# Kernel optimization log

Hardware: AMD Instinct MI355X
Metric: run time of the kernel (lower is better)

The kernel has to match this reference:

```python
import jax, jax.numpy as jnp
import numpy as np

N_QUBITS = 6
N_LAYERS = 2
QSVT_DEGREE = 3
DT_RANK = max(N_QUBITS // 2, 1)
OUT_DIM = 3 * N_QUBITS
PI = np.float32(np.pi)
DT_MIN, DT_MAX = 1e-3, 0.1
BATCH, SEQ = 256, 512


def _ry_mat(theta):
    c = jnp.cos(theta / 2)
    s = jnp.sin(theta / 2)
    row0 = jnp.stack([c, -s], axis=-1)
    row1 = jnp.stack([s, c], axis=-1)
    return jnp.stack([row0, row1], axis=-2).astype(jnp.complex64)


def _rz_mat(theta):
    e = jnp.exp(-0.5j * theta.astype(jnp.complex64))
    z = jnp.zeros_like(e)
    row0 = jnp.stack([e, z], axis=-1)
    row1 = jnp.stack([z, jnp.conj(e)], axis=-1)
    return jnp.stack([row0, row1], axis=-2)


def _rx_mat(theta):
    c = jnp.cos(theta / 2).astype(jnp.complex64)
    s = jnp.sin(theta / 2).astype(jnp.complex64)
    row0 = jnp.stack([c, -1j * s], axis=-1)
    row1 = jnp.stack([-1j * s, c], axis=-1)
    return jnp.stack([row0, row1], axis=-2)


def _apply1(state, mat, w):
    # state: (B, 2, ..., 2) tensor over N_QUBITS axes; mat: (2,2) or batched (B,2,2)
    state = jnp.moveaxis(state, 1 + w, -1)
    if mat.ndim == 3:
        state = jnp.einsum('bij,b...j->b...i', mat, state)
    else:
        state = jnp.einsum('ij,b...j->b...i', mat, state)
    return jnp.moveaxis(state, -1, 1 + w)


def _cnot(state, c, t):
    state = jnp.moveaxis(state, (1 + c, 1 + t), (-2, -1))
    state = state.at[..., 1, :].set(state[..., 1, ::-1])
    return jnp.moveaxis(state, (-2, -1), (1 + c, 1 + t))


def _crx(state, theta, c, t):
    state = jnp.moveaxis(state, (1 + c, 1 + t), (-2, -1))
    m = _rx_mat(theta)
    state = state.at[..., 1, :].set(jnp.einsum('ij,...j->...i', m, state[..., 1, :]))
    return jnp.moveaxis(state, (-2, -1), (1 + c, 1 + t))


def _circuit(h, x, dt, circuit_params, poly_coeffs, qsvt_params):
    """Batched statevector simulation of the selective QSVT + unified ansatz qnode."""
    n = N_QUBITS
    B = h.shape[0]
    state = jnp.zeros((B,) + (2,) * n, jnp.complex64)
    state = state.at[(slice(None),) + (0,) * n].set(1.0 + 0.0j)
    # 1) state encoding RY(h[t-1])
    for i in range(n):
        state = _apply1(state, _ry_mat(h[:, i]), i)
    # 2) Delta-modulated QSVT: RZ rotations + bidirectional CNOT ring per degree
    qidx = 0
    n_qp = n * QSVT_DEGREE
    for deg in range(QSVT_DEGREE + 1):
        coeff = poly_coeffs[deg]
        for i in range(n):
            if qidx < n_qp:
                ang = coeff * dt[:, i] * qsvt_params[qidx] * PI
                qidx += 1
            else:
                ang = coeff * dt[:, i] * PI
            state = _apply1(state, _rz_mat(ang), i)
        for i in range(n - 1):
            state = _cnot(state, i, i + 1)
        state = _cnot(state, n - 1, 0)
        for i in range(n - 1, 0, -1):
            state = _cnot(state, i, i - 1)
    # 3) unified variational ansatz
    p = 0
    for _ in range(N_LAYERS):
        for i in range(n):
            state = _apply1(state, _rx_mat(circuit_params[p]), i)
            state = _apply1(state, _ry_mat(circuit_params[p + 1]), i)
            state = _apply1(state, _rz_mat(circuit_params[p + 2]), i)
            p += 3
        for i in range(n):
            state = _crx(state, circuit_params[p], i, (i + 1) % n)
            p += 1
        for i in range(n - 1, -1, -1):
            state = _crx(state, circuit_params[p], i, (i - 1) % n)
            p += 1
    # 4) Delta-modulated input RY(x * dt)
    for i in range(n):
        state = _apply1(state, _ry_mat(x[:, i] * dt[:, i]), i)
    # 5) Pauli X/Y/Z expectation values per qubit
    xs, ys, zs = [], [], []
    for i in range(n):
        s = jnp.moveaxis(state, 1 + i, 1).reshape(B, 2, -1)
        z = jnp.sum(jnp.conj(s[:, 0]) * s[:, 1], axis=-1)
        xs.append(2.0 * jnp.real(z))
        ys.append(2.0 * jnp.imag(z))
        zs.append(jnp.sum(jnp.abs(s[:, 0]) ** 2 - jnp.abs(s[:, 1]) ** 2, axis=-1))
    return jnp.stack(xs + ys + zs, axis=-1).astype(jnp.float32)  # (B, 3n)


def setup_inputs() -> dict:
    key = jax.random.key(0)
    ks = jax.random.split(key, 8)
    angles = jax.random.uniform(ks[0], (BATCH, SEQ, N_QUBITS), jnp.float32) * PI
    Wx = jax.random.normal(ks[1], (DT_RANK + 2 * N_QUBITS, N_QUBITS), jnp.float32) / np.float32(np.sqrt(N_QUBITS))
    Wdt = jax.random.normal(ks[2], (N_QUBITS, DT_RANK), jnp.float32) / np.float32(np.sqrt(DT_RANK))
    dt = jnp.exp(jax.random.uniform(ks[3], (N_QUBITS,), jnp.float32) * np.float32(np.log(DT_MAX) - np.log(DT_MIN)) + np.float32(np.log(DT_MIN)))
    bdt = dt + jnp.log(-jnp.expm1(-dt))
    poly_coeffs = jax.random.normal(ks[4], (QSVT_DEGREE + 1,), jnp.float32) * 0.1
    qsvt_params = jax.random.normal(ks[5], (N_QUBITS * QSVT_DEGREE,), jnp.float32) * 0.1
    circuit_params = jax.random.normal(ks[6], (5 * N_QUBITS * N_LAYERS,), jnp.float32) * 0.1
    D = jnp.ones((OUT_DIM,), jnp.float32)
    Wc = jax.random.normal(ks[7], (OUT_DIM, N_QUBITS), jnp.float32) / np.float32(np.sqrt(N_QUBITS))
    return {"angles": angles, "Wx": Wx, "Wdt": Wdt, "bdt": bdt, "poly_coeffs": poly_coeffs, "qsvt_params": qsvt_params, "circuit_params": circuit_params, "D": D, "Wc": Wc}


def reference(angles, Wx, Wdt, bdt, poly_coeffs, qsvt_params, circuit_params, D, Wc):
    x_dbc = angles @ Wx.T  # (B,S, dt_rank + 2n)
    dt_raw = x_dbc[..., :DT_RANK]
    # B slice computed in the original but never used in forward
    C = x_dbc[..., DT_RANK + N_QUBITS:]
    dt_angles = jnp.tanh(jax.nn.softplus(dt_raw @ Wdt.T + bdt)) * PI  # (B,S,n)
    # quantum part is detached in the original (detach().cpu() before the qnode)
    sg = jax.lax.stop_gradient
    xs = (jnp.moveaxis(sg(angles), 1, 0), jnp.moveaxis(sg(dt_angles), 1, 0))
    cp, pc, qp = sg(circuit_params), sg(poly_coeffs), sg(qsvt_params)
    h0 = jnp.zeros((angles.shape[0], N_QUBITS), jnp.float32)

    def step(h, xt):
        x_t, dt_t = xt
        meas = _circuit(h, x_t, dt_t, cp, pc, qp)
        return meas[:, 2 * N_QUBITS:], meas  # carry = PauliZ block

    _, meas = jax.lax.scan(step, h0, xs)
    h_full = jnp.moveaxis(meas, 0, 1)  # (B,S,3n)
    return (C @ Wc.T) * h_full + D * jnp.concatenate([angles] * 3, axis=-1)
```

## Files before the change

### kernel.cpp

```cpp
#include <hip/hip_runtime.h>
#include <math.h>

#define BATCH 256
#define SEQ 512
#define SDS 54
#define PI_F 3.14159265358979323846f

template<int CTRL>
__device__ __forceinline__ float fdpp(float v) {
    return __int_as_float(__builtin_amdgcn_mov_dpp(__float_as_int(v), CTRL, 0xF, 0xF, true));
}
template<int L>
__device__ __forceinline__ float rdl(float v) {
    return __int_as_float(__builtin_amdgcn_readlane(__float_as_int(v), L));
}
__device__ __forceinline__ float rdlv(float v, int l) {
    return __int_as_float(__builtin_amdgcn_readlane(__float_as_int(v), l));
}
template<int M>
__device__ __forceinline__ float shxm(float v) {
    if constexpr (M == 1)       return fdpp<0xB1>(v);
    else if constexpr (M == 2)  return fdpp<0x4E>(v);
    else if constexpr (M == 8)  return fdpp<0x128>(v);
    else if constexpr (M == 32) return __shfl_xor(v, 32, 64);
    else return __int_as_float(__builtin_amdgcn_ds_swizzle(__float_as_int(v), (M << 10) | 0x1F));
}
__device__ __forceinline__ float redsum64(float v) {
    v += fdpp<0x128>(v);
    v += fdpp<0x124>(v);
    v += fdpp<0x122>(v);
    v += fdpp<0x121>(v);
    return (rdl<0>(v) + rdl<16>(v)) + (rdl<32>(v) + rdl<48>(v));
}
__device__ __forceinline__ float xorf(float v, int m) {
    return __int_as_float(__float_as_int(v) ^ m);
}
__device__ __forceinline__ void wg_barrier_lds() {
    __builtin_amdgcn_sched_barrier(0);
    __builtin_amdgcn_s_waitcnt(0xC07F);
    __builtin_amdgcn_s_barrier();
    __builtin_amdgcn_sched_barrier(0);
}
__device__ __forceinline__ int permf(int x) {
    const int cs[11] = {0,1,2,3,4,5,5,4,3,2,1};
    const int ts[11] = {1,2,3,4,5,0,4,3,2,1,0};
#pragma unroll
    for (int k = 10; k >= 0; k--) {
        int cb = (x >> (5 - cs[k])) & 1;
        x ^= cb << (5 - ts[k]);
    }
    return x;
}
__device__ __forceinline__ void cmul4(const float* c,
    float vr, float vi, float ar, float ai, float br, float bi, float cr, float ci,
    float& nr, float& ni) {
    nr = c[0]*vr - c[1]*vi + c[2]*ar - c[3]*ai + c[4]*br - c[5]*bi + c[6]*cr - c[7]*ci;
    ni = c[0]*vi + c[1]*vr + c[2]*ai + c[3]*ar + c[4]*bi + c[5]*br + c[6]*ci + c[7]*cr;
}
__device__ __forceinline__ void ringapply(const float* rc,
    float vr, float vi, float br, float bi, float cr, float ci, float dr, float di,
    float& nr, float& ni) {
    nr = rc[0]*vr - rc[1]*bi - rc[2]*ci + rc[3]*dr;
    ni = rc[0]*vi + rc[1]*br + rc[2]*cr + rc[3]*di;
}

__global__ __launch_bounds__(256) void prep_kernel(
    const float* __restrict__ angles, const float* __restrict__ Wx,
    const float* __restrict__ Wdt, const float* __restrict__ bdt,
    const float* __restrict__ D, const float* __restrict__ Wc,
    float* __restrict__ sd)
{
    int gid = blockIdx.x * blockDim.x + threadIdx.x;
    if (gid >= BATCH * SEQ) return;
    const float* a = angles + (size_t)gid * 6;
    float ang[6];
#pragma unroll
    for (int i = 0; i < 6; i++) ang[i] = a[i];
    float dtr[3];
#pragma unroll
    for (int r = 0; r < 3; r++) {
        float s = 0.f;
#pragma unroll
        for (int k = 0; k < 6; k++) s += ang[k] * Wx[r * 6 + k];
        dtr[r] = s;
    }
    float* rec = sd + (size_t)gid * SDS;
    float dtv[6];
#pragma unroll
    for (int i = 0; i < 6; i++) {
        float x = bdt[i];
#pragma unroll
        for (int r = 0; r < 3; r++) x += dtr[r] * Wdt[i * 3 + r];
        float sp = (x > 15.f) ? x : log1pf(expf(x));
        dtv[i] = tanhf(sp) * PI_F;
        rec[i] = dtv[i];
        float th = ang[i] * dtv[i];
        rec[6 + i]  = cosf(th);
        rec[12 + i] = sinf(th);
    }
    float C[6];
#pragma unroll
    for (int i = 0; i < 6; i++) {
        float s = 0.f;
#pragma unroll
        for (int k = 0; k < 6; k++) s += ang[k] * Wx[(9 + i) * 6 + k];
        C[i] = s;
    }
#pragma unroll
    for (int j = 0; j < 18; j++) {
        float s = 0.f;
#pragma unroll
        for (int i = 0; i < 6; i++) s += C[i] * Wc[j * 6 + i];
        rec[18 + j] = s;
        rec[36 + j] = D[j] * ang[j % 6];
    }
}

__global__ __launch_bounds__(64) void umat_kernel(const float* __restrict__ cp,
                                                  float2* __restrict__ um)
{
    const int lane = threadIdx.x;
    const int col = blockIdx.x;
    int bitv[6];
#pragma unroll
    for (int i = 0; i < 6; i++) bitv[i] = (lane >> (5 - i)) & 1;

    float qc[2][3][8], rc[2][6][4];
#pragma unroll
    for (int l = 0; l < 2; l++) {
        float g00r[6], g00i[6], g01r[6], g01i[6], g10r[6], g10i[6], g11r[6], g11i[6];
#pragma unroll
        for (int i = 0; i < 6; i++) {
            float ax = cp[l * 30 + i * 3 + 0];
            float ay = cp[l * 30 + i * 3 + 1];
            float az = cp[l * 30 + i * 3 + 2];
            float ca = cosf(0.5f * ax), sa = sinf(0.5f * ax);
            float cb = cosf(0.5f * ay), sb = sinf(0.5f * ay);
            float cg = cosf(0.5f * az), sg = sinf(0.5f * az);
            float m00r = cb * ca, m00i =  sb * sa;
            float m01r = -sb * ca, m01i = -cb * sa;
            float m10r =  sb * ca, m10i = -cb * sa;
            float m11r =  cb * ca, m11i = -sb * sa;
            g00r[i] = cg * m00r + sg * m00i; g00i[i] = cg * m00i - sg * m00r;
            g01r[i] = cg * m01r + sg * m01i; g01i[i] = cg * m01i - sg * m01r;
            g10r[i] = cg * m10r - sg * m10i; g10i[i] = cg * m10i + sg * m10r;
            g11r[i] = cg * m11r - sg * m11i; g11i[i] = cg * m11i + sg * m11r;
        }
#pragma unroll
        for (int pp = 0; pp < 3; pp++) {
            int aq = 2 * pp, bq = 2 * pp + 1;
            float dar = bitv[aq] ? g11r[aq] : g00r[aq], dai = bitv[aq] ? g11i[aq] : g00i[aq];
            float oar = bitv[aq] ? g10r[aq] : g01r[aq], oai = bitv[aq] ? g10i[aq] : g01i[aq];
            float dbr = bitv[bq] ? g11r[bq] : g00r[bq], dbi = bitv[bq] ? g11i[bq] : g00i[bq];
            float obr = bitv[bq] ? g10r[bq] : g01r[bq], obi = bitv[bq] ? g10i[bq] : g01i[bq];
            qc[l][pp][0] = dar * dbr - dai * dbi;  qc[l][pp][1] = dar * dbi + dai * dbr;
            qc[l][pp][2] = oar * dbr - oai * dbi;  qc[l][pp][3] = oar * dbi + oai * dbr;
            qc[l][pp][4] = dar * obr - dai * obi;  qc[l][pp][5] = dar * obi + dai * obr;
            qc[l][pp][6] = oar * obr - oai * obi;  qc[l][pp][7] = oar * obi + oai * obr;
        }
        const int Aq[6] = {0, 2, 4, 5, 3, 1};
        const int Bq[6] = {1, 3, 5, 4, 2, 0};
#pragma unroll
        for (int o = 0; o < 6; o++) {
            float tha = (o < 3) ? cp[l * 30 + 18 + 2 * o]     : cp[l * 30 + 24 + 2 * (o - 3)];
            float thb = (o < 3) ? cp[l * 30 + 18 + 2 * o + 1] : cp[l * 30 + 24 + 2 * (o - 3) + 1];
            float ca = cosf(0.5f * tha), sa = sinf(0.5f * tha);
            float cb = cosf(0.5f * thb), sb = sinf(0.5f * thb);
            int ba = bitv[Aq[o]], bb = bitv[Bq[o]];
            float mx0 = ba ? ca : 1.f, sae = ba ? sa : 0.f;
            float ny0 = bb ? cb : 1.f, sbe = bb ? sb : 0.f;
            rc[l][o][0] = ny0 * mx0; rc[l][o][1] = -ny0 * sae;
            rc[l][o][2] = -mx0 * sbe; rc[l][o][3] = -sae * sbe;
        }
    }

    float re = (lane == col) ? 1.f : 0.f;
    float im = 0.f;
    auto p1q = [&](int mi, int mj, const float* c) {
        float ar = __shfl_xor(re, mi, 64), ai = __shfl_xor(im, mi, 64);
        float br = __shfl_xor(re, mj, 64), bi = __shfl_xor(im, mj, 64);
        float cr = __shfl_xor(re, mi | mj, 64), ci = __shfl_xor(im, mi | mj, 64);
        float nr, ni;
        cmul4(c, re, im, ar, ai, br, bi, cr, ci, nr, ni);
        re = nr; im = ni;
    };
    auto rng = [&](int mb, int mc, const float* c) {
        float br = __shfl_xor(re, mb, 64), bi = __shfl_xor(im, mb, 64);
        float cr = __shfl_xor(re, mc, 64), ci = __shfl_xor(im, mc, 64);
        float dr = __shfl_xor(re, mb | mc, 64), di = __shfl_xor(im, mb | mc, 64);
        float nr, ni;
        ringapply(c, re, im, br, bi, cr, ci, dr, di, nr, ni);
        re = nr; im = ni;
    };
#pragma unroll
    for (int l = 0; l < 2; l++) {
        p1q(32, 16, qc[l][0]);
        p1q(8, 4, qc[l][1]);
        p1q(2, 1, qc[l][2]);
        rng(16, 8, rc[l][0]);
        rng(4, 2, rc[l][1]);
        rng(1, 32, rc[l][2]);
        rng(2, 4, rc[l][3]);
        rng(8, 16, rc[l][4]);
        rng(32, 1, rc[l][5]);
    }
    um[(size_t)lane * 64 + col] = make_float2(re, im);
}

__global__ __launch_bounds__(256, 1) void step_kernel(
    const float* __restrict__ sd, const float* __restrict__ pc,
    const float* __restrict__ qp, const float2* __restrict__ um,
    float* __restrict__ out)
{
    __shared__ float2 sPart[2][4][64];
    const int tid = threadIdx.x;
    const int wave = tid >> 6;
    const int lane = tid & 63;
    const int b = blockIdx.x;

    int bitv[6];
#pragma unroll
    for (int i = 0; i < 6; i++) bitv[i] = (lane >> (5 - i)) & 1;
    int sflip[6];
#pragma unroll
    for (int q = 0; q < 6; q++) sflip[q] = bitv[q] ? (int)0x80000000 : 0;

    const int jbase = wave * 16;
    float2 row[16];
#pragma unroll
    for (int jj = 0; jj < 16; jj++) row[jj] = um[(size_t)lane * 64 + jbase + jj];

    float A[6], sel[6];
    {
        int x1 = permf(lane), x2 = permf(x1), x3 = permf(x2), x4 = permf(x3);
#pragma unroll
        for (int i = 0; i < 6; i++) {
            float u0 = pc[0] * PI_F * qp[0 * 6 + i];
            float u1 = pc[1] * PI_F * qp[1 * 6 + i];
            float u2 = pc[2] * PI_F * qp[2 * 6 + i];
            float u3 = pc[3] * PI_F;
            float t1 = ((x1 >> (5 - i)) & 1) ? 0.5f : -0.5f;
            float t2 = ((x2 >> (5 - i)) & 1) ? 0.5f : -0.5f;
            float t3 = ((x3 >> (5 - i)) & 1) ? 0.5f : -0.5f;
            float t4 = ((x4 >> (5 - i)) & 1) ? 0.5f : -0.5f;
            A[i] = u3 * t1 + u2 * t2 + u1 * t3 + u0 * t4;
            sel[i] = (float)((x4 >> (5 - i)) & 1);
        }
    }

    const float* sdb = sd + (size_t)b * SEQ * SDS;
    float* outb = out + (size_t)b * SEQ * 18;

    float h0 = 0.f, h1 = 0.f, h2 = 0.f, h3 = 0.f, h4 = 0.f, h5 = 0.f;
    float ysv[6], pX[6];
#pragma unroll
    for (int q = 0; q < 6; q++) { ysv[q] = 0.f; pX[q] = 0.f; }

    float cd[18], nd[18];
#pragma unroll
    for (int k = 0; k < 18; k++) cd[k] = sdb[k];

    for (int t = 0; t < SEQ; t++) {
        const float* r  = sdb + (size_t)t * SDS;
        const float* rn = sdb + (size_t)((t + 1 < SEQ) ? t + 1 : t) * SDS;
#pragma unroll
        for (int k = 0; k < 18; k++) nd[k] = rn[k];

        if (wave == 3 && t > 0) {
            const float* rp = sdb + (size_t)(t - 1) * SDS;
            float* o = outb + (size_t)(t - 1) * 18;
            float Y0 = redsum64(ysv[0]), Y1 = redsum64(ysv[1]), Y2 = redsum64(ysv[2]);
            float Y3 = redsum64(ysv[3]), Y4 = redsum64(ysv[4]), Y5 = redsum64(ysv[5]);
            if (lane == 0) {
                float Yv[6] = {Y0, Y1, Y2, Y3, Y4, Y5};
#pragma unroll
                for (int q = 0; q < 6; q++) {
                    o[q]     = fmaf(rp[18 + q], pX[q], rp[36 + q]);
                    o[6 + q] = fmaf(rp[24 + q], Yv[q], rp[42 + q]);
                }
            }
        }

        float phi = A[0]*cd[0] + A[1]*cd[1] + A[2]*cd[2] + A[3]*cd[3] + A[4]*cd[4] + A[5]*cd[5];
        float sph, cph;
        __sincosf(phi, &sph, &cph);

        float ss0, cc0, ss1, cc1, ss2, cc2, ss3, cc3, ss4, cc4, ss5, cc5;
        __sincosf(0.5f * h0, &ss0, &cc0);
        __sincosf(0.5f * h1, &ss1, &cc1);
        __sincosf(0.5f * h2, &ss2, &cc2);
        __sincosf(0.5f * h3, &ss3, &cc3);
        __sincosf(0.5f * h4, &ss4, &cc4);
        __sincosf(0.5f * h5, &ss5, &cc5);
        float f0 = fmaf(sel[0], ss0 - cc0, cc0);
        float f1 = fmaf(sel[1], ss1 - cc1, cc1);
        float f2 = fmaf(sel[2], ss2 - cc2, cc2);
        float f3 = fmaf(sel[3], ss3 - cc3, cc3);
        float f4 = fmaf(sel[4], ss4 - cc4, cc4);
        float f5 = fmaf(sel[5], ss5 - cc5, cc5);
        float prod = ((f0 * f1) * (f2 * f3)) * (f4 * f5);
        float pr = prod * cph, pi = prod * sph;

        float ar0 = 0.f, ai0 = 0.f, ar1 = 0.f, ai1 = 0.f;
#pragma unroll
        for (int jj = 0; jj < 16; jj += 2) {
            float sr0 = rdlv(pr, jbase + jj);
            float si0 = rdlv(pi, jbase + jj);
            float sr1 = rdlv(pr, jbase + jj + 1);
            float si1 = rdlv(pi, jbase + jj + 1);
            ar0 = fmaf(row[jj].x, sr0, ar0);
            ar0 = fmaf(-row[jj].y, si0, ar0);
            ai0 = fmaf(row[jj].x, si0, ai0);
            ai0 = fmaf(row[jj].y, sr0, ai0);
            ar1 = fmaf(row[jj + 1].x, sr1, ar1);
            ar1 = fmaf(-row[jj + 1].y, si1, ar1);
            ai1 = fmaf(row[jj + 1].x, si1, ai1);
            ai1 = fmaf(row[jj + 1].y, sr1, ai1);
        }
        sPart[t & 1][wave][lane] = make_float2(ar0 + ar1, ai0 + ai1);
        wg_barrier_lds();
        float2 q0v = sPart[t & 1][0][lane], q1v = sPart[t & 1][1][lane];
        float2 q2v = sPart[t & 1][2][lane], q3v = sPart[t & 1][3][lane];
        float re = (q0v.x + q1v.x) + (q2v.x + q3v.x);
        float im = (q0v.y + q1v.y) + (q2v.y + q3v.y);

        float p = re * re + im * im;
        float g0r = shxm<32>(re), g0i = shxm<32>(im);
        float g1r = shxm<16>(re), g1i = shxm<16>(im);
        float g2r = shxm<8>(re),  g2i = shxm<8>(im);
        float g3r = shxm<4>(re),  g3i = shxm<4>(im);
        float g4r = shxm<2>(re),  g4i = shxm<2>(im);
        float g5r = shxm<1>(re),  g5i = shxm<1>(im);

        float Z0 = redsum64(xorf(p, sflip[0]));
        float Z1 = redsum64(xorf(p, sflip[1]));
        float Z2 = redsum64(xorf(p, sflip[2]));
        float Z3 = redsum64(xorf(p, sflip[3]));
        float Z4 = redsum64(xorf(p, sflip[4]));
        float Z5 = redsum64(xorf(p, sflip[5]));
        float X0 = redsum64(fmaf(re, g0r, im * g0i));
        float X1 = redsum64(fmaf(re, g1r, im * g1i));
        float X2 = redsum64(fmaf(re, g2r, im * g2i));
        float X3 = redsum64(fmaf(re, g3r, im * g3i));
        float X4 = redsum64(fmaf(re, g4r, im * g4i));
        float X5 = redsum64(fmaf(re, g5r, im * g5i));

        h0 = cd[6]  * Z0 - cd[12] * X0;
        h1 = cd[7]  * Z1 - cd[13] * X1;
        h2 = cd[8]  * Z2 - cd[14] * X2;
        h3 = cd[9]  * Z3 - cd[15] * X3;
        h4 = cd[10] * Z4 - cd[16] * X4;
        h5 = cd[11] * Z5 - cd[17] * X5;

        if (wave == 0 && lane == 0) {
            float* o = outb + (size_t)t * 18;
            float hh[6] = {h0, h1, h2, h3, h4, h5};
#pragma unroll
            for (int q = 0; q < 6; q++) o[12 + q] = fmaf(r[30 + q], hh[q], r[48 + q]);
        }
        if (wave == 3) {
            ysv[0] = xorf(re * g0i - im * g0r, sflip[0]);
            ysv[1] = xorf(re * g1i - im * g1r, sflip[1]);
            ysv[2] = xorf(re * g2i - im * g2r, sflip[2]);
            ysv[3] = xorf(re * g3i - im * g3r, sflip[3]);
            ysv[4] = xorf(re * g4i - im * g4r, sflip[4]);
            ysv[5] = xorf(re * g5i - im * g5r, sflip[5]);
            float Zv[6] = {Z0, Z1, Z2, Z3, Z4, Z5};
            float Xv[6] = {X0, X1, X2, X3, X4, X5};
#pragma unroll
            for (int q = 0; q < 6; q++) pX[q] = cd[6 + q] * Xv[q] + cd[12 + q] * Zv[q];
        }

#pragma unroll
        for (int k = 0; k < 18; k++) cd[k] = nd[k];
    }

    if (wave == 3) {
        const float* rp = sdb + (size_t)(SEQ - 1) * SDS;
        float* o = outb + (size_t)(SEQ - 1) * 18;
        float Y0 = redsum64(ysv[0]), Y1 = redsum64(ysv[1]), Y2 = redsum64(ysv[2]);
        float Y3 = redsum64(ysv[3]), Y4 = redsum64(ysv[4]), Y5 = redsum64(ysv[5]);
        if (lane == 0) {
            float Yv[6] = {Y0, Y1, Y2, Y3, Y4, Y5};
#pragma unroll
            for (int q = 0; q < 6; q++) {
                o[q]     = fmaf(rp[18 + q], pX[q], rp[36 + q]);
                o[6 + q] = fmaf(rp[24 + q], Yv[q], rp[42 + q]);
            }
        }
    }
}

extern "C" void kernel_launch(void* const* d_in, const int* in_sizes, int n_in,
                              void* d_out, int out_size, void* d_ws, size_t ws_size,
                              hipStream_t stream) {
    const float* angles = (const float*)d_in[0];
    const float* Wx     = (const float*)d_in[1];
    const float* Wdt    = (const float*)d_in[2];
    const float* bdt    = (const float*)d_in[3];
    const float* pc     = (const float*)d_in[4];
    const float* qp     = (const float*)d_in[5];
    const float* cp     = (const float*)d_in[6];
    const float* D      = (const float*)d_in[7];
    const float* Wc     = (const float*)d_in[8];
    float* sd  = (float*)d_ws;
    float2* um = (float2*)(sd + (size_t)BATCH * SEQ * SDS);
    float* out = (float*)d_out;

    umat_kernel<<<64, 64, 0, stream>>>(cp, um);
    prep_kernel<<<(BATCH * SEQ) / 256, 256, 0, stream>>>(angles, Wx, Wdt, bdt, D, Wc, sd);
    step_kernel<<<BATCH, 256, 0, stream>>>(sd, pc, qp, um, out);
}
```

Baseline: 801.7 us.

## Split Z/X reductions across waves via LDS and use native sin/cos

Each of the four waves now computes only a share of the twelve Z/X wave reductions and writes it to shared memory. A second barrier then lets every wave read all twelve values, where before every wave computed all twelve redundantly on the serial critical path. The output epilogue coefficients are prefetched into registers one step ahead instead of being reloaded from global memory at store time. The sincos calls are replaced with the hardware sin/cos instructions on pre-scaled inputs. The trade-off is an extra workgroup barrier per timestep, a single-buffered partial array, and possibly lower precision for large angles.

```diff
diff --git a/kernel.cpp b/kernel.cpp
--- a/kernel.cpp
+++ b/kernel.cpp
@@ -5,6 +5,7 @@
 #define SEQ 512
 #define SDS 54
 #define PI_F 3.14159265358979323846f
+#define INV2PI 0.15915494309189535f
 
 template<int CTRL>
 __device__ __forceinline__ float fdpp(float v) {
@@ -34,6 +35,11 @@
 }
 __device__ __forceinline__ float xorf(float v, int m) {
     return __int_as_float(__float_as_int(v) ^ m);
+}
+__device__ __forceinline__ void nsincos(float x, float& s, float& c) {
+    float r = x * INV2PI;
+    s = __builtin_amdgcn_sinf(r);
+    c = __builtin_amdgcn_cosf(r);
 }
 __device__ __forceinline__ void wg_barrier_lds() {
     __builtin_amdgcn_sched_barrier(0);
@@ -212,7 +218,8 @@
     const float* __restrict__ qp, const float2* __restrict__ um,
     float* __restrict__ out)
 {
-    __shared__ float2 sPart[2][4][64];
+    __shared__ float2 sPart[4][64];
+    __shared__ __align__(16) float sZX[12];
     const int tid = threadIdx.x;
     const int wave = tid >> 6;
     const int lane = tid & 63;
@@ -252,46 +259,62 @@
     float* outb = out + (size_t)b * SEQ * 18;
 
     float h0 = 0.f, h1 = 0.f, h2 = 0.f, h3 = 0.f, h4 = 0.f, h5 = 0.f;
-    float ysv[6], pX[6];
-#pragma unroll
-    for (int q = 0; q < 6; q++) { ysv[q] = 0.f; pX[q] = 0.f; }
 
     float cd[18], nd[18];
+    float zf[12], zfn[12];
+    float wf[24], wfn[24], pwf[24];
+    float ysv[6], px[6];
+#pragma unroll
+    for (int q = 0; q < 6; q++) { ysv[q] = 0.f; px[q] = 0.f; }
 #pragma unroll
     for (int k = 0; k < 18; k++) cd[k] = sdb[k];
+    if (wave == 0) {
+#pragma unroll
+        for (int j = 0; j < 6; j++) { zf[j] = sdb[30 + j]; zf[6 + j] = sdb[48 + j]; }
+    }
+    if (wave == 3) {
+#pragma unroll
+        for (int j = 0; j < 12; j++) { wf[j] = sdb[18 + j]; wf[12 + j] = sdb[36 + j]; }
+    }
 
     for (int t = 0; t < SEQ; t++) {
-        const float* r  = sdb + (size_t)t * SDS;
         const float* rn = sdb + (size_t)((t + 1 < SEQ) ? t + 1 : t) * SDS;
 #pragma unroll
         for (int k = 0; k < 18; k++) nd[k] = rn[k];
+        if (wave == 0) {
+#pragma unroll
+            for (int j = 0; j < 6; j++) { zfn[j] = rn[30 + j]; zfn[6 + j] = rn[48 + j]; }
+        }
+        if (wave == 3) {
+#pragma unroll
+            for (int j = 0; j < 12; j++) { wfn[j] = rn[18 + j]; wfn[12 + j] = rn[36 + j]; }
+        }
 
         if (wave == 3 && t > 0) {
-            const float* rp = sdb + (size_t)(t - 1) * SDS;
-            float* o = outb + (size_t)(t - 1) * 18;
             float Y0 = redsum64(ysv[0]), Y1 = redsum64(ysv[1]), Y2 = redsum64(ysv[2]);
             float Y3 = redsum64(ysv[3]), Y4 = redsum64(ysv[4]), Y5 = redsum64(ysv[5]);
             if (lane == 0) {
                 float Yv[6] = {Y0, Y1, Y2, Y3, Y4, Y5};
+                float* o = outb + (size_t)(t - 1) * 18;
 #pragma unroll
                 for (int q = 0; q < 6; q++) {
-                    o[q]     = fmaf(rp[18 + q], pX[q], rp[36 + q]);
-                    o[6 + q] = fmaf(rp[24 + q], Yv[q], rp[42 + q]);
+                    o[q]     = fmaf(pwf[q],     px[q], pwf[12 + q]);
+                    o[6 + q] = fmaf(pwf[6 + q], Yv[q], pwf[18 + q]);
                 }
             }
         }
 
         float phi = A[0]*cd[0] + A[1]*cd[1] + A[2]*cd[2] + A[3]*cd[3] + A[4]*cd[4] + A[5]*cd[5];
         float sph, cph;
-        __sincosf(phi, &sph, &cph);
+        nsincos(phi, sph, cph);
 
         float ss0, cc0, ss1, cc1, ss2, cc2, ss3, cc3, ss4, cc4, ss5, cc5;
-        __sincosf(0.5f * h0, &ss0, &cc0);
-        __sincosf(0.5f * h1, &ss1, &cc1);
-        __sincosf(0.5f * h2, &ss2, &cc2);
-        __sincosf(0.5f * h3, &ss3, &cc3);
-        __sincosf(0.5f * h4, &ss4, &cc4);
-        __sincosf(0.5f * h5, &ss5, &cc5);
+        nsincos(0.5f * h0, ss0, cc0);
+        nsincos(0.5f * h1, ss1, cc1);
+        nsincos(0.5f * h2, ss2, cc2);
+        nsincos(0.5f * h3, ss3, cc3);
+        nsincos(0.5f * h4, ss4, cc4);
+        nsincos(0.5f * h5, ss5, cc5);
         float f0 = fmaf(sel[0], ss0 - cc0, cc0);
         float f1 = fmaf(sel[1], ss1 - cc1, cc1);
         float f2 = fmaf(sel[2], ss2 - cc2, cc2);
@@ -317,75 +340,100 @@
             ai1 = fmaf(row[jj + 1].x, si1, ai1);
             ai1 = fmaf(row[jj + 1].y, sr1, ai1);
         }
-        sPart[t & 1][wave][lane] = make_float2(ar0 + ar1, ai0 + ai1);
+        sPart[wave][lane] = make_float2(ar0 + ar1, ai0 + ai1);
         wg_barrier_lds();
-        float2 q0v = sPart[t & 1][0][lane], q1v = sPart[t & 1][1][lane];
-        float2 q2v = sPart[t & 1][2][lane], q3v = sPart[t & 1][3][lane];
+        float2 q0v = sPart[0][lane], q1v = sPart[1][lane];
+        float2 q2v = sPart[2][lane], q3v = sPart[3][lane];
         float re = (q0v.x + q1v.x) + (q2v.x + q3v.x);
         float im = (q0v.y + q1v.y) + (q2v.y + q3v.y);
 
-        float p = re * re + im * im;
-        float g0r = shxm<32>(re), g0i = shxm<32>(im);
-        float g1r = shxm<16>(re), g1i = shxm<16>(im);
-        float g2r = shxm<8>(re),  g2i = shxm<8>(im);
-        float g3r = shxm<4>(re),  g3i = shxm<4>(im);
-        float g4r = shxm<2>(re),  g4i = shxm<2>(im);
-        float g5r = shxm<1>(re),  g5i = shxm<1>(im);
-
-        float Z0 = redsum64(xorf(p, sflip[0]));
-        float Z1 = redsum64(xorf(p, sflip[1]));
-        float Z2 = redsum64(xorf(p, sflip[2]));
-        float Z3 = redsum64(xorf(p, sflip[3]));
-        float Z4 = redsum64(xorf(p, sflip[4]));
-        float Z5 = redsum64(xorf(p, sflip[5]));
-        float X0 = redsum64(fmaf(re, g0r, im * g0i));
-        float X1 = redsum64(fmaf(re, g1r, im * g1i));
-        float X2 = redsum64(fmaf(re, g2r, im * g2i));
-        float X3 = redsum64(fmaf(re, g3r, im * g3i));
-        float X4 = redsum64(fmaf(re, g4r, im * g4i));
-        float X5 = redsum64(fmaf(re, g5r, im * g5i));
-
-        h0 = cd[6]  * Z0 - cd[12] * X0;
-        h1 = cd[7]  * Z1 - cd[13] * X1;
-        h2 = cd[8]  * Z2 - cd[14] * X2;
-        h3 = cd[9]  * Z3 - cd[15] * X3;
-        h4 = cd[10] * Z4 - cd[16] * X4;
-        h5 = cd[11] * Z5 - cd[17] * X5;
-
-        if (wave == 0 && lane == 0) {
-            float* o = outb + (size_t)t * 18;
-            float hh[6] = {h0, h1, h2, h3, h4, h5};
-#pragma unroll
-            for (int q = 0; q < 6; q++) o[12 + q] = fmaf(r[30 + q], hh[q], r[48 + q]);
-        }
-        if (wave == 3) {
+        if (wave == 0) {
+            float p = re * re + im * im;
+            float Z0 = redsum64(xorf(p, sflip[0]));
+            float Z1 = redsum64(xorf(p, sflip[1]));
+            float Z2 = redsum64(xorf(p, sflip[2]));
+            float Z3 = redsum64(xorf(p, sflip[3]));
+            if (lane == 0) { sZX[0] = Z0; sZX[1] = Z1; sZX[2] = Z2; sZX[3] = Z3; }
+        } else if (wave == 1) {
+            float p = re * re + im * im;
+            float Z4 = redsum64(xorf(p, sflip[4]));
+            float Z5 = redsum64(xorf(p, sflip[5]));
+            float g0r = shxm<32>(re), g0i = shxm<32>(im);
+            float g1r = shxm<16>(re), g1i = shxm<16>(im);
+            float X0 = redsum64(fmaf(re, g0r, im * g0i));
+            float X1 = redsum64(fmaf(re, g1r, im * g1i));
+            if (lane == 0) { sZX[4] = Z4; sZX[5] = Z5; sZX[6] = X0; sZX[7] = X1; }
+        } else if (wave == 2) {
+            float g2r = shxm<8>(re), g2i = shxm<8>(im);
+            float g3r = shxm<4>(re), g3i = shxm<4>(im);
+            float g4r = shxm<2>(re), g4i = shxm<2>(im);
+            float g5r = shxm<1>(re), g5i = shxm<1>(im);
+            float X2 = redsum64(fmaf(re, g2r, im * g2i));
+            float X3 = redsum64(fmaf(re, g3r, im * g3i));
+            float X4 = redsum64(fmaf(re, g4r, im * g4i));
+            float X5 = redsum64(fmaf(re, g5r, im * g5i));
+            if (lane == 0) { sZX[8] = X2; sZX[9] = X3; sZX[10] = X4; sZX[11] = X5; }
+        } else {
+            float g0r = shxm<32>(re), g0i = shxm<32>(im);
+            float g1r = shxm<16>(re), g1i = shxm<16>(im);
+            float g2r = shxm<8>(re),  g2i = shxm<8>(im);
+            float g3r = shxm<4>(re),  g3i = shxm<4>(im);
+            float g4r = shxm<2>(re),  g4i = shxm<2>(im);
+            float g5r = shxm<1>(re),  g5i = shxm<1>(im);
             ysv[0] = xorf(re * g0i - im * g0r, sflip[0]);
             ysv[1] = xorf(re * g1i - im * g1r, sflip[1]);
             ysv[2] = xorf(re * g2i - im * g2r, sflip[2]);
             ysv[3] = xorf(re * g3i - im * g3r, sflip[3]);
             ysv[4] = xorf(re * g4i - im * g4r, sflip[4]);
             ysv[5] = xorf(re * g5i - im * g5r, sflip[5]);
-            float Zv[6] = {Z0, Z1, Z2, Z3, Z4, Z5};
-            float Xv[6] = {X0, X1, X2, X3, X4, X5};
-#pragma unroll
-            for (int q = 0; q < 6; q++) pX[q] = cd[6 + q] * Xv[q] + cd[12 + q] * Zv[q];
+        }
+        wg_barrier_lds();
+
+        float4 v0 = ((const float4*)sZX)[0];
+        float4 v1 = ((const float4*)sZX)[1];
+        float4 v2 = ((const float4*)sZX)[2];
+        float Zv[6] = {v0.x, v0.y, v0.z, v0.w, v1.x, v1.y};
+        float Xv[6] = {v1.z, v1.w, v2.x, v2.y, v2.z, v2.w};
+        h0 = cd[6]  * Zv[0] - cd[12] * Xv[0];
+        h1 = cd[7]  * Zv[1] - cd[13] * Xv[1];
+        h2 = cd[8]  * Zv[2] - cd[14] * Xv[2];
+        h3 = cd[9]  * Zv[3] - cd[15] * Xv[3];
+        h4 = cd[10] * Zv[4] - cd[16] * Xv[4];
+        h5 = cd[11] * Zv[5] - cd[17] * Xv[5];
+
+        if (wave == 0 && lane == 0) {
+            float* o = outb + (size_t)t * 18;
+            float hh[6] = {h0, h1, h2, h3, h4, h5};
+#pragma unroll
+            for (int q = 0; q < 6; q++) o[12 + q] = fmaf(zf[q], hh[q], zf[6 + q]);
+        }
+        if (wave == 3) {
+#pragma unroll
+            for (int q = 0; q < 6; q++) px[q] = cd[6 + q] * Xv[q] + cd[12 + q] * Zv[q];
         }
 
 #pragma unroll
         for (int k = 0; k < 18; k++) cd[k] = nd[k];
+        if (wave == 0) {
+#pragma unroll
+            for (int k = 0; k < 12; k++) zf[k] = zfn[k];
+        }
+        if (wave == 3) {
+#pragma unroll
+            for (int k = 0; k < 24; k++) { pwf[k] = wf[k]; wf[k] = wfn[k]; }
+        }
     }
 
     if (wave == 3) {
-        const float* rp = sdb + (size_t)(SEQ - 1) * SDS;
-        float* o = outb + (size_t)(SEQ - 1) * 18;
         float Y0 = redsum64(ysv[0]), Y1 = redsum64(ysv[1]), Y2 = redsum64(ysv[2]);
         float Y3 = redsum64(ysv[3]), Y4 = redsum64(ysv[4]), Y5 = redsum64(ysv[5]);
         if (lane == 0) {
             float Yv[6] = {Y0, Y1, Y2, Y3, Y4, Y5};
+            float* o = outb + (size_t)(SEQ - 1) * 18;
 #pragma unroll
             for (int q = 0; q < 6; q++) {
-                o[q]     = fmaf(rp[18 + q], pX[q], rp[36 + q]);
-                o[6 + q] = fmaf(rp[24 + q], Yv[q], rp[42 + q]);
+                o[q]     = fmaf(pwf[q],     px[q], pwf[12 + q]);
+                o[6 + q] = fmaf(pwf[6 + q], Yv[q], pwf[18 + q]);
             }
         }
     }
```

After: 1.006 ms. 1.25x slower.
